# Performance work log

Measured on AMD Instinct MI355X. Metric: run time of the kernel, lower is better.

## Reference

```python
import jax, jax.numpy as jnp
import numpy as np

N_NODES = 100000
N_EDGES = 3200000
DIM_IN = 256
DIM_OUT = 256


def setup_inputs() -> dict:
    key = jax.random.key(0)
    k1, k2, k3, k4, k5 = jax.random.split(key, 5)
    x = jax.random.normal(k1, (N_NODES, DIM_IN), dtype=jnp.float32)
    adj_rows = jax.random.randint(k2, (N_EDGES,), 0, N_NODES, dtype=jnp.int64)
    adj_cols = jax.random.randint(k3, (N_EDGES,), 0, N_NODES, dtype=jnp.int64)
    adj_vals = jax.random.uniform(k4, (N_EDGES,), dtype=jnp.float32)
    # torch Linear weight: [dim_out, dim_in]
    W = jax.random.normal(k5, (DIM_OUT, DIM_IN), dtype=jnp.float32) * (1.0 / np.sqrt(DIM_IN))
    return {"x": x, "adj_rows": adj_rows, "adj_cols": adj_cols, "adj_vals": adj_vals, "W": W}


def reference(x, adj_rows, adj_cols, adj_vals, W):
    # h = Linear(x) with no bias -> x @ W.T  : [N, dim_out]
    h = jnp.einsum('nd,od->no', x, W)
    # sparse.mm(adjacency, h): out[r] = sum_{edges e with row r} val[e] * h[col[e]]
    msgs = adj_vals[:, None] * h[adj_cols]            # [E, dim_out]
    out = jax.ops.segment_sum(msgs, adj_rows, num_segments=N_NODES)
    return out
```

## Files before the change

### kernel.cpp

```cpp
#include <hip/hip_runtime.h>
#include <hip/hip_bf16.h>

#define DIM 256
#define GRP 4
#define CAP8 56
#define OVF_CAP 65536

typedef short s16x8 __attribute__((ext_vector_type(8)));
typedef float f32x4 __attribute__((ext_vector_type(4)));

__device__ inline unsigned short f32_bf16_rne(float f) {
    unsigned u = __float_as_uint(f);
    u += 0x7FFFu + ((u >> 16) & 1u);
    return (unsigned short)(u >> 16);
}
__device__ inline float bf16_f32(unsigned short h) {
    return __uint_as_float(((unsigned)h) << 16);
}
__device__ inline float4 bf16x4_f32(uint2 p) {
    float4 r;
    r.x = __uint_as_float(p.x << 16);
    r.y = __uint_as_float(p.x & 0xFFFF0000u);
    r.z = __uint_as_float(p.y << 16);
    r.w = __uint_as_float(p.y & 0xFFFF0000u);
    return r;
}

__global__ __launch_bounds__(256) void prep_w(const float* __restrict__ W,
                                              unsigned short* __restrict__ Wh) {
    int i = blockIdx.x * 256 + threadIdx.x;
    Wh[i] = f32_bf16_rne(W[i]);
}

__global__ __launch_bounds__(256) void gemm_mfma(const float* __restrict__ X,
                                                 const unsigned short* __restrict__ Wh,
                                                 unsigned short* __restrict__ H, int N) {
    __shared__ __align__(16) unsigned short xh[64 * 32];
    __shared__ __align__(16) unsigned short xl[64 * 32];

    const int tid = threadIdx.x;
    const int lane = tid & 63;
    const int wv = tid >> 6;
    const int bm = blockIdx.x * 64;

    const int srow = tid & 63;
    const int schunk = tid >> 6;
    const int grow = bm + srow;
    const bool rowok = grow < N;
    const float* xsrc = X + (size_t)grow * DIM + schunk * 8;
    const int swch = srow * 4 + (schunk ^ ((srow >> 1) & 3));

    const int frow = lane & 15;
    const int fch = lane >> 4;

    f32x4 acc[4][4] = {};

    for (int k0 = 0; k0 < DIM; k0 += 32) {
        float v[8];
        if (rowok) {
            float4 a = *(const float4*)(xsrc + k0);
            float4 b = *(const float4*)(xsrc + k0 + 4);
            v[0] = a.x; v[1] = a.y; v[2] = a.z; v[3] = a.w;
            v[4] = b.x; v[5] = b.y; v[6] = b.z; v[7] = b.w;
        } else {
#pragma unroll
            for (int e = 0; e < 8; ++e) v[e] = 0.f;
        }
        unsigned hh[8], ll[8];
#pragma unroll
        for (int e = 0; e < 8; ++e) {
            unsigned short hu = f32_bf16_rne(v[e]);
            hh[e] = hu;
            ll[e] = f32_bf16_rne(v[e] - bf16_f32(hu));
        }
        uint4 hv = make_uint4(hh[0] | (hh[1] << 16), hh[2] | (hh[3] << 16),
                              hh[4] | (hh[5] << 16), hh[6] | (hh[7] << 16));
        uint4 lv = make_uint4(ll[0] | (ll[1] << 16), ll[2] | (ll[3] << 16),
                              ll[4] | (ll[5] << 16), ll[6] | (ll[7] << 16));
        ((uint4*)xh)[swch] = hv;
        ((uint4*)xl)[swch] = lv;
        __syncthreads();

        s16x8 ah[4], al[4], bh[4];
#pragma unroll
        for (int i = 0; i < 4; ++i) {
            int row = i * 16 + frow;
            int rch = row * 4 + (fch ^ ((row >> 1) & 3));
            ah[i] = __builtin_bit_cast(s16x8, ((const uint4*)xh)[rch]);
            al[i] = __builtin_bit_cast(s16x8, ((const uint4*)xl)[rch]);
        }
#pragma unroll
        for (int j = 0; j < 4; ++j) {
            size_t off = (size_t)(wv * 64 + j * 16 + frow) * DIM + k0 + fch * 8;
            bh[j] = __builtin_bit_cast(s16x8, *(const uint4*)(Wh + off));
        }
#pragma unroll
        for (int i = 0; i < 4; ++i)
#pragma unroll
            for (int j = 0; j < 4; ++j) {
                acc[i][j] = __builtin_amdgcn_mfma_f32_16x16x32_bf16(ah[i], bh[j], acc[i][j], 0, 0, 0);
                acc[i][j] = __builtin_amdgcn_mfma_f32_16x16x32_bf16(al[i], bh[j], acc[i][j], 0, 0, 0);
            }
        __syncthreads();
    }

#pragma unroll
    for (int i = 0; i < 4; ++i)
#pragma unroll
        for (int r = 0; r < 4; ++r) {
            int row = bm + i * 16 + fch * 4 + r;
            if (row < N) {
#pragma unroll
                for (int j = 0; j < 4; ++j)
                    H[(size_t)row * DIM + wv * 64 + j * 16 + frow] = f32_bf16_rne(acc[i][j][r]);
            }
        }
}

__global__ __launch_bounds__(256) void scatter_bucket4(const int* __restrict__ rows,
                                                       const int* __restrict__ cols,
                                                       const float* __restrict__ vals,
                                                       int* __restrict__ cur,
                                                       unsigned long long* __restrict__ buckets,
                                                       uint4* __restrict__ ovf,
                                                       int* __restrict__ ovf_cnt,
                                                       int nE, int B4) {
    unsigned xcd;
    asm volatile("s_getreg_b32 %0, hwreg(HW_REG_XCC_ID)" : "=s"(xcd));
    xcd &= 7;

    int i = blockIdx.x * 256 + threadIdx.x;
    int st = gridDim.x * 256;
    for (int e = i; e < nE; e += st) {
        int r = rows[e];
        unsigned c = (unsigned)cols[e];
        unsigned vb = __float_as_uint(vals[e]);
        int cell = (int)xcd * B4 + (r >> 2);
        int p = atomicAdd(&cur[cell], 1);
        if (p < CAP8) {
            unsigned lo = c | ((unsigned)(r & 3) << 17);
            buckets[(size_t)cell * CAP8 + p] = (unsigned long long)lo | ((unsigned long long)vb << 32);
        } else {
            int q = atomicAdd(ovf_cnt, 1);
            if (q < OVF_CAP) ovf[q] = make_uint4((unsigned)r, c, vb, 0u);
        }
    }
}

__global__ __launch_bounds__(256) void bucket_agg4(const unsigned short* __restrict__ hb,
                                                   const unsigned long long* __restrict__ buckets,
                                                   const int* __restrict__ cur,
                                                   float* __restrict__ out, int N, int B4) {
    const int lane = threadIdx.x & 63;
    const int g = (blockIdx.x * 256 + threadIdx.x) >> 6;
    if (g >= B4) return;

    f32x4 a0 = {0,0,0,0}, a1 = {0,0,0,0}, a2 = {0,0,0,0}, a3 = {0,0,0,0};

#define ACCUM(e, gth)                                                        \
    {                                                                        \
        float vv = __uint_as_float((unsigned)((e) >> 32));                   \
        int idx = (int)(((unsigned)(e) >> 17) & 3u);                         \
        float4 f = bf16x4_f32(gth);                                          \
        f32x4 d = {vv * f.x, vv * f.y, vv * f.z, vv * f.w};                  \
        switch (idx) {                                                       \
            case 0: a0 += d; break;  case 1: a1 += d; break;                 \
            case 2: a2 += d; break;  default: a3 += d; break;                \
        }                                                                    \
    }

    for (int x = 0; x < 8; ++x) {
        const int cell = x * B4 + g;
        const int cnt = min(cur[cell], CAP8);
        const unsigned long long* p = buckets + (size_t)cell * CAP8;

        int j = 0;
        for (; j + 8 <= cnt; j += 8) {
            unsigned long long e0 = __builtin_nontemporal_load(p + j);
            unsigned long long e1 = __builtin_nontemporal_load(p + j + 1);
            unsigned long long e2 = __builtin_nontemporal_load(p + j + 2);
            unsigned long long e3 = __builtin_nontemporal_load(p + j + 3);
            unsigned long long e4 = __builtin_nontemporal_load(p + j + 4);
            unsigned long long e5 = __builtin_nontemporal_load(p + j + 5);
            unsigned long long e6 = __builtin_nontemporal_load(p + j + 6);
            unsigned long long e7 = __builtin_nontemporal_load(p + j + 7);
            uint2 g0 = *(const uint2*)(hb + (size_t)((unsigned)e0 & 0x1FFFFu) * DIM + lane * 4);
            uint2 g1 = *(const uint2*)(hb + (size_t)((unsigned)e1 & 0x1FFFFu) * DIM + lane * 4);
            uint2 g2 = *(const uint2*)(hb + (size_t)((unsigned)e2 & 0x1FFFFu) * DIM + lane * 4);
            uint2 g3 = *(const uint2*)(hb + (size_t)((unsigned)e3 & 0x1FFFFu) * DIM + lane * 4);
            uint2 g4 = *(const uint2*)(hb + (size_t)((unsigned)e4 & 0x1FFFFu) * DIM + lane * 4);
            uint2 g5 = *(const uint2*)(hb + (size_t)((unsigned)e5 & 0x1FFFFu) * DIM + lane * 4);
            uint2 g6 = *(const uint2*)(hb + (size_t)((unsigned)e6 & 0x1FFFFu) * DIM + lane * 4);
            uint2 g7 = *(const uint2*)(hb + (size_t)((unsigned)e7 & 0x1FFFFu) * DIM + lane * 4);
            ACCUM(e0, g0) ACCUM(e1, g1) ACCUM(e2, g2) ACCUM(e3, g3)
            ACCUM(e4, g4) ACCUM(e5, g5) ACCUM(e6, g6) ACCUM(e7, g7)
        }
        for (; j < cnt; ++j) {
            unsigned long long e = __builtin_nontemporal_load(p + j);
            uint2 gv = *(const uint2*)(hb + (size_t)((unsigned)e & 0x1FFFFu) * DIM + lane * 4);
            ACCUM(e, gv)
        }
    }
#undef ACCUM

    const int r0 = g * GRP;
#define STORE_ROW(i, acc) \
    { int r = r0 + (i); if (r < N) __builtin_nontemporal_store(acc, (f32x4*)(out + (size_t)r * DIM + lane * 4)); }
    STORE_ROW(0, a0) STORE_ROW(1, a1) STORE_ROW(2, a2) STORE_ROW(3, a3)
#undef STORE_ROW
}

__global__ __launch_bounds__(256) void ovf_fix(const unsigned short* __restrict__ hb,
                                               const uint4* __restrict__ ovf,
                                               const int* __restrict__ ovf_cnt,
                                               float* __restrict__ out) {
    const int n = min(*ovf_cnt, OVF_CAP);
    const int lane = threadIdx.x & 63;
    const int w = (blockIdx.x * 256 + threadIdx.x) >> 6;
    const int nw = gridDim.x * 4;
    for (int e = w; e < n; e += nw) {
        uint4 t = ovf[e];
        float vv = __uint_as_float(t.z);
        float4 f = bf16x4_f32(*(const uint2*)(hb + (size_t)t.y * DIM + lane * 4));
        float* op = out + (size_t)t.x * DIM + lane * 4;
        atomicAdd(op + 0, vv * f.x);
        atomicAdd(op + 1, vv * f.y);
        atomicAdd(op + 2, vv * f.z);
        atomicAdd(op + 3, vv * f.w);
    }
}

__global__ __launch_bounds__(256) void edge_scatter(const unsigned short* __restrict__ hb,
                                                    const int* __restrict__ rows,
                                                    const int* __restrict__ cols,
                                                    const float* __restrict__ vals,
                                                    float* __restrict__ out, int nE) {
    const int lane = threadIdx.x & 63;
    const int wave = (blockIdx.x * blockDim.x + threadIdx.x) >> 6;
    const int nWaves = (gridDim.x * blockDim.x) >> 6;
    for (int e = wave; e < nE; e += nWaves) {
        const int r = rows[e];
        const int c = cols[e];
        const float v = vals[e];
        float4 f = bf16x4_f32(*(const uint2*)(hb + (size_t)c * DIM + lane * 4));
        float* op = out + (size_t)r * DIM + lane * 4;
        atomicAdd(op + 0, v * f.x);
        atomicAdd(op + 1, v * f.y);
        atomicAdd(op + 2, v * f.z);
        atomicAdd(op + 3, v * f.w);
    }
}

extern "C" void kernel_launch(void* const* d_in, const int* in_sizes, int n_in,
                              void* d_out, int out_size, void* d_ws, size_t ws_size,
                              hipStream_t stream) {
    const float* x    = (const float*)d_in[0];
    const int*   rows = (const int*)d_in[1];
    const int*   cols = (const int*)d_in[2];
    const float* vals = (const float*)d_in[3];
    const float* W    = (const float*)d_in[4];

    float* out = (float*)d_out;
    const int N  = in_sizes[0] / DIM;
    const int nE = in_sizes[1];
    const int B4 = (N + GRP - 1) / GRP;
    const int cells = 8 * B4;

    auto align256 = [](size_t v) { return (v + 255) & ~(size_t)255; };
    char* ws = (char*)d_ws;

    size_t off_wh   = 0;
    size_t off_h    = align256(off_wh + (size_t)DIM * DIM * 2);
    size_t off_cur  = align256(off_h + (size_t)N * DIM * 2);
    size_t off_ovf  = align256(off_cur + (size_t)(cells + 64) * 4);
    size_t off_bkt  = align256(off_ovf + (size_t)OVF_CAP * 16);
    size_t total    = off_bkt + (size_t)cells * CAP8 * 8;

    unsigned short* Wh = (unsigned short*)(ws + off_wh);
    unsigned short* h  = (unsigned short*)(ws + off_h);

    const bool packOK = (N <= (1 << 17));

    prep_w<<<DIM * DIM / 256, 256, 0, stream>>>(W, Wh);

    if (ws_size >= total && packOK) {
        int*   cur     = (int*)(ws + off_cur);
        int*   ovf_cnt = cur + cells;
        uint4* ovf     = (uint4*)(ws + off_ovf);
        unsigned long long* bkt = (unsigned long long*)(ws + off_bkt);

        hipMemsetAsync(cur, 0, (size_t)(cells + 64) * 4, stream);
        scatter_bucket4<<<2048, 256, 0, stream>>>(rows, cols, vals, cur, bkt, ovf, ovf_cnt, nE, B4);

        gemm_mfma<<<(N + 63) / 64, 256, 0, stream>>>(x, Wh, h, N);

        bucket_agg4<<<(B4 + 3) / 4, 256, 0, stream>>>(h, bkt, cur, out, N, B4);
        ovf_fix<<<32, 256, 0, stream>>>(h, ovf, ovf_cnt, out);
    } else {
        gemm_mfma<<<(N + 63) / 64, 256, 0, stream>>>(x, Wh, h, N);
        hipMemsetAsync(out, 0, (size_t)out_size * sizeof(float), stream);
        edge_scatter<<<2048, 256, 0, stream>>>(h, rows, cols, vals, out, nE);
    }
}
```

Baseline: 522.5 us.

## Fuse edge bucketing and MFMA GEMM into one launch to overlap them

Merges the atomic edge-bucketing scatter and the bf16 MFMA projection GEMM into a single kernel, split by block index. The first 2048 blocks bucket edges and the remaining blocks compute row tiles of h. The aim is to overlap the latency-bound atomic scatter with the compute- and bandwidth-bound GEMM and to save a launch gap. In exchange, every block now reserves the GEMM's shared memory and the register budget of the heavier path, which can lower scatter occupancy.

```diff
diff --git a/kernel.cpp b/kernel.cpp
--- a/kernel.cpp
+++ b/kernel.cpp
@@ -5,6 +5,7 @@
 #define GRP 4
 #define CAP8 56
 #define OVF_CAP 65536
+#define NSCAT 2048
 
 typedef short s16x8 __attribute__((ext_vector_type(8)));
 typedef float f32x4 __attribute__((ext_vector_type(4)));
@@ -32,16 +33,14 @@
     Wh[i] = f32_bf16_rne(W[i]);
 }
 
-__global__ __launch_bounds__(256) void gemm_mfma(const float* __restrict__ X,
-                                                 const unsigned short* __restrict__ Wh,
-                                                 unsigned short* __restrict__ H, int N) {
-    __shared__ __align__(16) unsigned short xh[64 * 32];
-    __shared__ __align__(16) unsigned short xl[64 * 32];
-
+__device__ __forceinline__ void gemm_body(const float* __restrict__ X,
+                                          const unsigned short* __restrict__ Wh,
+                                          unsigned short* __restrict__ H, int N, int gb,
+                                          unsigned short* xh, unsigned short* xl) {
     const int tid = threadIdx.x;
     const int lane = tid & 63;
     const int wv = tid >> 6;
-    const int bm = blockIdx.x * 64;
+    const int bm = gb * 64;
 
     const int srow = tid & 63;
     const int schunk = tid >> 6;
@@ -117,20 +116,20 @@
         }
 }
 
-__global__ __launch_bounds__(256) void scatter_bucket4(const int* __restrict__ rows,
-                                                       const int* __restrict__ cols,
-                                                       const float* __restrict__ vals,
-                                                       int* __restrict__ cur,
-                                                       unsigned long long* __restrict__ buckets,
-                                                       uint4* __restrict__ ovf,
-                                                       int* __restrict__ ovf_cnt,
-                                                       int nE, int B4) {
+__device__ __forceinline__ void scatter_body(const int* __restrict__ rows,
+                                             const int* __restrict__ cols,
+                                             const float* __restrict__ vals,
+                                             int* __restrict__ cur,
+                                             unsigned long long* __restrict__ buckets,
+                                             uint4* __restrict__ ovf,
+                                             int* __restrict__ ovf_cnt,
+                                             int nE, int B4, int sb) {
     unsigned xcd;
     asm volatile("s_getreg_b32 %0, hwreg(HW_REG_XCC_ID)" : "=s"(xcd));
     xcd &= 7;
 
-    int i = blockIdx.x * 256 + threadIdx.x;
-    int st = gridDim.x * 256;
+    int i = sb * 256 + threadIdx.x;
+    int st = NSCAT * 256;
     for (int e = i; e < nE; e += st) {
         int r = rows[e];
         unsigned c = (unsigned)cols[e];
@@ -145,6 +144,35 @@
             if (q < OVF_CAP) ovf[q] = make_uint4((unsigned)r, c, vb, 0u);
         }
     }
+}
+
+__global__ __launch_bounds__(256) void fused_sg(const float* __restrict__ X,
+                                                const unsigned short* __restrict__ Wh,
+                                                unsigned short* __restrict__ H,
+                                                const int* __restrict__ rows,
+                                                const int* __restrict__ cols,
+                                                const float* __restrict__ vals,
+                                                int* __restrict__ cur,
+                                                unsigned long long* __restrict__ buckets,
+                                                uint4* __restrict__ ovf,
+                                                int* __restrict__ ovf_cnt,
+                                                int N, int nE, int B4) {
+    __shared__ __align__(16) unsigned short xh[64 * 32];
+    __shared__ __align__(16) unsigned short xl[64 * 32];
+
+    if (blockIdx.x < NSCAT) {
+        scatter_body(rows, cols, vals, cur, buckets, ovf, ovf_cnt, nE, B4, blockIdx.x);
+    } else {
+        gemm_body(X, Wh, H, N, blockIdx.x - NSCAT, xh, xl);
+    }
+}
+
+__global__ __launch_bounds__(256) void gemm_mfma(const float* __restrict__ X,
+                                                 const unsigned short* __restrict__ Wh,
+                                                 unsigned short* __restrict__ H, int N) {
+    __shared__ __align__(16) unsigned short xh[64 * 32];
+    __shared__ __align__(16) unsigned short xl[64 * 32];
+    gemm_body(X, Wh, H, N, blockIdx.x, xh, xl);
 }
 
 __global__ __launch_bounds__(256) void bucket_agg4(const unsigned short* __restrict__ hb,
@@ -290,9 +318,10 @@
         unsigned long long* bkt = (unsigned long long*)(ws + off_bkt);
 
         hipMemsetAsync(cur, 0, (size_t)(cells + 64) * 4, stream);
-        scatter_bucket4<<<2048, 256, 0, stream>>>(rows, cols, vals, cur, bkt, ovf, ovf_cnt, nE, B4);
-
-        gemm_mfma<<<(N + 63) / 64, 256, 0, stream>>>(x, Wh, h, N);
+
+        const int nGemm = (N + 63) / 64;
+        fused_sg<<<NSCAT + nGemm, 256, 0, stream>>>(x, Wh, h, rows, cols, vals,
+                                                    cur, bkt, ovf, ovf_cnt, N, nE, B4);
 
         bucket_agg4<<<(B4 + 3) / 4, 256, 0, stream>>>(h, bkt, cur, out, N, B4);
         ovf_fix<<<32, 256, 0, stream>>>(h, ovf, ovf_cnt, out);
```

Result: faster. 491.6 us (-5.9%).
